# Kernel tuning notes

Hardware: AMD Instinct MI355X
Metric: run time of the kernel (lower is better)

Reference implementation:

```python
import jax, jax.numpy as jnp
import numpy as np

N_NODES = 50000
N_PAIRS = 800000
D = 64          # node feature dim
N_BASIS = 8     # basis functions per pair


def setup_inputs() -> dict:
    key = jax.random.key(0)
    k1, k2, k3, k4, k5, k6 = jax.random.split(key, 6)
    p1 = jax.random.normal(k1, (N_NODES, D), dtype=jnp.float32)
    pair_i = jax.random.randint(k2, (N_PAIRS,), 0, N_NODES, dtype=jnp.int64)
    pair_j = jax.random.randint(k3, (N_PAIRS,), 0, N_NODES, dtype=jnp.int64)
    basis = jax.random.normal(k4, (N_PAIRS, N_BASIS), dtype=jnp.float32)
    # bias-free MLP: 64 -> 256 -> 512 (= D * N_BASIS), scaled init
    W1 = jax.random.normal(k5, (D, 256), dtype=jnp.float32) / np.sqrt(D)
    W2 = jax.random.normal(k6, (256, D * N_BASIS), dtype=jnp.float32) / np.sqrt(256.0)
    return {"p1": p1, "pair_i": pair_i, "pair_j": pair_j, "basis": basis,
            "W1": W1, "W2": W2}


def reference(p1, pair_i, pair_j, basis, W1, W2):
    # gather node features for both ends of each pair and sum -> [n_pairs, D]
    inter = p1[pair_i] + p1[pair_j]
    # bias-free FeedForward with tanh between layers
    h = jnp.tanh(inter @ W1)          # [n_pairs, 256]
    h = h @ W2                        # [n_pairs, D * N_BASIS]
    h = h.reshape(-1, p1.shape[-1], basis.shape[-1])  # [n_pairs, D, n_basis]
    out = jnp.einsum('icb,ib->ic', h, basis)          # [n_pairs, D]
    return out[:, None, :]            # [n_pairs, 1, D]
```

## Files before the change

kernel.cpp:

```cpp
#include <hip/hip_runtime.h>

typedef unsigned short u16;
typedef unsigned int   u32;
typedef __bf16 bf16x8 __attribute__((ext_vector_type(8)));
typedef float  f32x4  __attribute__((ext_vector_type(4)));
typedef float  f32x2  __attribute__((ext_vector_type(2)));
typedef unsigned short u16x8 __attribute__((ext_vector_type(8)));

#define PPB 160

__device__ __forceinline__ u16 f2bf(float f){
  union { float f; u32 i; } v; v.f = f;
  u32 u = v.i;
  u += 0x7fffu + ((u >> 16) & 1u);
  return (u16)(u >> 16);
}
__device__ __forceinline__ float tanh_fast(float x){
  x = fminf(fmaxf(x, -12.f), 12.f);
  float t = __builtin_amdgcn_exp2f(x * 2.885390081777926815f);
  return (t - 1.f) * __builtin_amdgcn_rcpf(t + 1.f);
}

__global__ __launch_bounds__(256) void transpose_cast_k(
    const float* __restrict__ in, u16* __restrict__ out, int R, int C)
{
  __shared__ u16 tile[64][65];
  const int tx = threadIdx.x & 63;
  const int ty = threadIdx.x >> 6;
  const int c0 = blockIdx.x * 64;
  const int r0 = blockIdx.y * 64;
#pragma unroll
  for (int rr = 0; rr < 16; ++rr){
    int r = ty + rr * 4;
    tile[r][tx] = f2bf(in[(size_t)(r0 + r) * C + c0 + tx]);
  }
  __syncthreads();
#pragma unroll
  for (int rr = 0; rr < 16; ++rr){
    int r = ty + rr * 4;
    out[(size_t)(c0 + r) * R + r0 + tx] = tile[tx][r];
  }
}

__global__ __launch_bounds__(256) void w2_block_k(
    const float* __restrict__ in, u16* __restrict__ out)
{
  __shared__ float tile[32][65];
  const int kk = blockIdx.x;
  const int n0 = blockIdx.y * 64;
  const int t  = threadIdx.x;
  {
    int r  = t >> 3;
    int c8 = t & 7;
    const float* src = in + (size_t)(kk*32 + r)*512 + n0 + c8*8;
    f32x4 v0 = *(const f32x4*)src;
    f32x4 v1 = *(const f32x4*)(src + 4);
#pragma unroll
    for (int e = 0; e < 4; ++e){
      tile[r][c8*8 + e]     = v0[e];
      tile[r][c8*8 + 4 + e] = v1[e];
    }
  }
  __syncthreads();
  {
    int c = t >> 2, part = t & 3;
    u16x8 o;
#pragma unroll
    for (int e = 0; e < 8; ++e) o[e] = f2bf(tile[part*8 + e][c]);
    *(u16x8*)(out + ((size_t)kk*512 + n0 + c)*32 + part*8) = o;
  }
}

__global__ __launch_bounds__(512, 2) void pilayer_kernel(
    const float* __restrict__ p1,
    const int* __restrict__ pair_i,
    const int* __restrict__ pair_j,
    const float* __restrict__ basis,
    const u16* __restrict__ w1t,
    const u16* __restrict__ w2b,
    float* __restrict__ out,
    int n_pairs)
{
  extern __shared__ __align__(16) u16 smem[];
  u16* sh_h     = smem;
  u16* sh_inter = smem + PPB * 264;

  const int tid  = threadIdx.x;
  const int blk  = blockIdx.x;
  const int lane = tid & 63;
  const int w    = tid >> 6;
  const int m16  = lane & 15;
  const int q    = lane >> 4;

  bf16x8 awf[8][4];
#pragma unroll
  for (int kk = 0; kk < 8; ++kk)
#pragma unroll
    for (int nt = 0; nt < 4; ++nt)
      awf[kk][nt] = *(const bf16x8*)(
          w2b + ((size_t)kk*512 + w*64 + nt*16 + m16)*32 + q*8);
  __builtin_amdgcn_sched_barrier(0);

  for (int u = tid; u < PPB * 4; u += 512){
    int m   = u >> 2;
    int seg = u & 3;
    int p   = blk * PPB + m;
    if (p >= n_pairs) p = n_pairs - 1;
    const f32x4* pi = (const f32x4*)(p1 + (size_t)pair_i[p] * 64 + seg * 16);
    const f32x4* pj = (const f32x4*)(p1 + (size_t)pair_j[p] * 64 + seg * 16);
    f32x4 a0 = pi[0], a1 = pi[1], a2 = pi[2], a3 = pi[3];
    f32x4 b0 = pj[0], b1 = pj[1], b2 = pj[2], b3 = pj[3];
    u16x8 r0, r1;
#pragma unroll
    for (int e = 0; e < 4; ++e){
      r0[e]     = f2bf(a0[e] + b0[e]);
      r0[e + 4] = f2bf(a1[e] + b1[e]);
      r1[e]     = f2bf(a2[e] + b2[e]);
      r1[e + 4] = f2bf(a3[e] + b3[e]);
    }
    u16x8* dst = (u16x8*)(sh_inter + m * 72 + seg * 16);
    dst[0] = r0; dst[1] = r1;
  }
  __syncthreads();

  {
    bf16x8 af[2][2];
#pragma unroll
    for (int nt1 = 0; nt1 < 2; ++nt1)
#pragma unroll
      for (int kh = 0; kh < 2; ++kh)
        af[nt1][kh] = *(const bf16x8*)(
            w1t + (size_t)(w*32 + nt1*16 + m16)*64 + kh*32 + q*8);

    for (int mt1 = 0; mt1 < PPB/16; ++mt1){
      const u16* irow = sh_inter + (mt1*16 + m16)*72 + q*8;
      bf16x8 b0 = *(const bf16x8*)(irow);
      bf16x8 b1 = *(const bf16x8*)(irow + 32);
#pragma unroll
      for (int nt1 = 0; nt1 < 2; ++nt1){
        f32x4 acc = {0.f, 0.f, 0.f, 0.f};
        acc = __builtin_amdgcn_mfma_f32_16x16x32_bf16(af[nt1][0], b0, acc, 0, 0, 0);
        acc = __builtin_amdgcn_mfma_f32_16x16x32_bf16(af[nt1][1], b1, acc, 0, 0, 0);
        u32 lo = (u32)f2bf(tanh_fast(acc[0])) | ((u32)f2bf(tanh_fast(acc[1])) << 16);
        u32 hi = (u32)f2bf(tanh_fast(acc[2])) | ((u32)f2bf(tanh_fast(acc[3])) << 16);
        u32* dst = (u32*)(sh_h + (size_t)(mt1*16 + m16)*264 + w*32 + nt1*16 + q*4);
        dst[0] = lo; dst[1] = hi;
      }
    }
  }
  __syncthreads();

  for (int mt = 0; mt < PPB/16; ++mt){
    const int mg  = blk * PPB + mt*16 + m16;
    const int mgc = (mg < n_pairs) ? mg : (n_pairs - 1);
    f32x4 bb = *(const f32x4*)(basis + (size_t)mgc*8 + (q & 1)*4);

    const u16* hrow = sh_h + (size_t)(mt*16 + m16)*264 + q*8;
    f32x4 acc[4];
#pragma unroll
    for (int nt = 0; nt < 4; ++nt) acc[nt] = (f32x4){0.f, 0.f, 0.f, 0.f};

    bf16x8 bh = *(const bf16x8*)(hrow);
#pragma unroll
    for (int kk = 0; kk < 8; ++kk){
      bf16x8 bhn;
      if (kk < 7) bhn = *(const bf16x8*)(hrow + (kk + 1)*32);
#pragma unroll
      for (int nt = 0; nt < 4; ++nt)
        acc[nt] = __builtin_amdgcn_mfma_f32_16x16x32_bf16(
            awf[kk][nt], bh, acc[nt], 0, 0, 0);
      bh = bhn;
    }

#pragma unroll
    for (int nt = 0; nt < 4; ++nt){
      f32x4 a = acc[nt];
      float s = a[0]*bb[0] + a[1]*bb[1] + a[2]*bb[2] + a[3]*bb[3];
      s += __shfl_xor(s, 16);
      float v2 = __shfl_xor(s, 32);
      if (q == 0 && mg < n_pairs){
        f32x2 pk = {s, v2};
        *(f32x2*)(out + (size_t)mg*64 + w*8 + nt*2) = pk;
      }
    }
  }
}

extern "C" void kernel_launch(void* const* d_in, const int* in_sizes, int n_in,
                              void* d_out, int out_size, void* d_ws, size_t ws_size,
                              hipStream_t stream)
{
  const float* p1    = (const float*)d_in[0];
  const int*   pi    = (const int*)d_in[1];
  const int*   pj    = (const int*)d_in[2];
  const float* basis = (const float*)d_in[3];
  const float* W1    = (const float*)d_in[4];
  const float* W2    = (const float*)d_in[5];
  float* out = (float*)d_out;

  u16* w1t = (u16*)d_ws;
  u16* w2b = w1t + 64 * 256;

  const int n_pairs = in_sizes[1];
  const int lds_bytes = (PPB * 264 + PPB * 72) * (int)sizeof(u16);

  static int attr_done = 0;
  if (!attr_done){
    hipFuncSetAttribute((const void*)pilayer_kernel,
                        hipFuncAttributeMaxDynamicSharedMemorySize, lds_bytes);
    attr_done = 1;
  }

  transpose_cast_k<<<dim3(4, 1), 256, 0, stream>>>(W1, w1t, 64, 256);
  w2_block_k<<<dim3(8, 8), 256, 0, stream>>>(W2, w2b);

  const int blocks = (n_pairs + PPB - 1) / PPB;
  pilayer_kernel<<<blocks, 512, lds_bytes, stream>>>(
      p1, pi, pj, basis, w1t, w2b, out, n_pairs);
}
```

Measured before the change: 615.4 us.

## Double block to 1024 threads, halve per-wave tiles, XOR-swizzle LDS

The fused kernel moves from 512 to 1024 threads per block. Each wave now owns half as many output columns in both GEMMs, so it holds 16 W2 fragments in registers instead of 32, and the launch bounds hint at higher occupancy. The LDS row padding (264/72) is replaced by an XOR swizzle on 16-byte chunks to avoid bank conflicts while shrinking shared memory. The trade-off is that every wave re-reads the same h and inter rows from LDS, giving more LDS traffic per MFMA, and the larger block adds scheduling pressure.

```diff
diff --git a/kernel.cpp b/kernel.cpp
--- a/kernel.cpp
+++ b/kernel.cpp
@@ -6,6 +6,7 @@
 typedef float  f32x4  __attribute__((ext_vector_type(4)));
 typedef float  f32x2  __attribute__((ext_vector_type(2)));
 typedef unsigned short u16x8 __attribute__((ext_vector_type(8)));
+typedef unsigned int   u32x2 __attribute__((ext_vector_type(2)));
 
 #define PPB 160
 
@@ -71,7 +72,7 @@
   }
 }
 
-__global__ __launch_bounds__(512, 2) void pilayer_kernel(
+__global__ __launch_bounds__(1024, 4) void pilayer_kernel(
     const float* __restrict__ p1,
     const int* __restrict__ pair_i,
     const int* __restrict__ pair_j,
@@ -83,7 +84,7 @@
 {
   extern __shared__ __align__(16) u16 smem[];
   u16* sh_h     = smem;
-  u16* sh_inter = smem + PPB * 264;
+  u16* sh_inter = smem + PPB * 256;
 
   const int tid  = threadIdx.x;
   const int blk  = blockIdx.x;
@@ -91,96 +92,85 @@
   const int w    = tid >> 6;
   const int m16  = lane & 15;
   const int q    = lane >> 4;
-
-  bf16x8 awf[8][4];
+  const int sw   = m16 & 7;
+
+  bf16x8 awf[8][2];
 #pragma unroll
   for (int kk = 0; kk < 8; ++kk)
 #pragma unroll
-    for (int nt = 0; nt < 4; ++nt)
+    for (int nt = 0; nt < 2; ++nt)
       awf[kk][nt] = *(const bf16x8*)(
-          w2b + ((size_t)kk*512 + w*64 + nt*16 + m16)*32 + q*8);
+          w2b + ((size_t)kk*512 + w*32 + nt*16 + m16)*32 + q*8);
   __builtin_amdgcn_sched_barrier(0);
 
-  for (int u = tid; u < PPB * 4; u += 512){
-    int m   = u >> 2;
-    int seg = u & 3;
+  for (int u = tid; u < PPB * 8; u += 1024){
+    int m   = u >> 3;
+    int seg = u & 7;
     int p   = blk * PPB + m;
     if (p >= n_pairs) p = n_pairs - 1;
-    const f32x4* pi = (const f32x4*)(p1 + (size_t)pair_i[p] * 64 + seg * 16);
-    const f32x4* pj = (const f32x4*)(p1 + (size_t)pair_j[p] * 64 + seg * 16);
-    f32x4 a0 = pi[0], a1 = pi[1], a2 = pi[2], a3 = pi[3];
-    f32x4 b0 = pj[0], b1 = pj[1], b2 = pj[2], b3 = pj[3];
-    u16x8 r0, r1;
+    const f32x4* pi = (const f32x4*)(p1 + (size_t)pair_i[p] * 64 + seg * 8);
+    const f32x4* pj = (const f32x4*)(p1 + (size_t)pair_j[p] * 64 + seg * 8);
+    f32x4 a0 = pi[0], a1 = pi[1];
+    f32x4 c0 = pj[0], c1 = pj[1];
+    u16x8 r;
 #pragma unroll
     for (int e = 0; e < 4; ++e){
-      r0[e]     = f2bf(a0[e] + b0[e]);
-      r0[e + 4] = f2bf(a1[e] + b1[e]);
-      r1[e]     = f2bf(a2[e] + b2[e]);
-      r1[e + 4] = f2bf(a3[e] + b3[e]);
-    }
-    u16x8* dst = (u16x8*)(sh_inter + m * 72 + seg * 16);
-    dst[0] = r0; dst[1] = r1;
+      r[e]     = f2bf(a0[e] + c0[e]);
+      r[e + 4] = f2bf(a1[e] + c1[e]);
+    }
+    *(u16x8*)(sh_inter + m * 64 + ((seg ^ (m & 7)) * 8)) = r;
   }
   __syncthreads();
 
   {
-    bf16x8 af[2][2];
-#pragma unroll
-    for (int nt1 = 0; nt1 < 2; ++nt1)
-#pragma unroll
-      for (int kh = 0; kh < 2; ++kh)
-        af[nt1][kh] = *(const bf16x8*)(
-            w1t + (size_t)(w*32 + nt1*16 + m16)*64 + kh*32 + q*8);
-
+    const u16* arow = w1t + (size_t)(w*16 + m16)*64 + q*8;
+    bf16x8 af0 = *(const bf16x8*)(arow);
+    bf16x8 af1 = *(const bf16x8*)(arow + 32);
+    const int cw = (w*2 + (q >> 1)) ^ sw;
     for (int mt1 = 0; mt1 < PPB/16; ++mt1){
-      const u16* irow = sh_inter + (mt1*16 + m16)*72 + q*8;
-      bf16x8 b0 = *(const bf16x8*)(irow);
-      bf16x8 b1 = *(const bf16x8*)(irow + 32);
-#pragma unroll
-      for (int nt1 = 0; nt1 < 2; ++nt1){
-        f32x4 acc = {0.f, 0.f, 0.f, 0.f};
-        acc = __builtin_amdgcn_mfma_f32_16x16x32_bf16(af[nt1][0], b0, acc, 0, 0, 0);
-        acc = __builtin_amdgcn_mfma_f32_16x16x32_bf16(af[nt1][1], b1, acc, 0, 0, 0);
-        u32 lo = (u32)f2bf(tanh_fast(acc[0])) | ((u32)f2bf(tanh_fast(acc[1])) << 16);
-        u32 hi = (u32)f2bf(tanh_fast(acc[2])) | ((u32)f2bf(tanh_fast(acc[3])) << 16);
-        u32* dst = (u32*)(sh_h + (size_t)(mt1*16 + m16)*264 + w*32 + nt1*16 + q*4);
-        dst[0] = lo; dst[1] = hi;
-      }
+      const u16* irow = sh_inter + (size_t)(mt1*16 + m16) * 64;
+      bf16x8 b0 = *(const bf16x8*)(irow + (q ^ sw) * 8);
+      bf16x8 b1 = *(const bf16x8*)(irow + ((q + 4) ^ sw) * 8);
+      f32x4 acc = {0.f, 0.f, 0.f, 0.f};
+      acc = __builtin_amdgcn_mfma_f32_16x16x32_bf16(af0, b0, acc, 0, 0, 0);
+      acc = __builtin_amdgcn_mfma_f32_16x16x32_bf16(af1, b1, acc, 0, 0, 0);
+      u32 lo = (u32)f2bf(tanh_fast(acc[0])) | ((u32)f2bf(tanh_fast(acc[1])) << 16);
+      u32 hi = (u32)f2bf(tanh_fast(acc[2])) | ((u32)f2bf(tanh_fast(acc[3])) << 16);
+      u32x2 pk = {lo, hi};
+      *(u32x2*)(sh_h + (size_t)(mt1*16 + m16)*256 + cw*8 + (q & 1)*4) = pk;
     }
   }
   __syncthreads();
 
   for (int mt = 0; mt < PPB/16; ++mt){
-    const int mg  = blk * PPB + mt*16 + m16;
+    const int row = mt*16 + m16;
+    const int mg  = blk * PPB + row;
     const int mgc = (mg < n_pairs) ? mg : (n_pairs - 1);
     f32x4 bb = *(const f32x4*)(basis + (size_t)mgc*8 + (q & 1)*4);
 
-    const u16* hrow = sh_h + (size_t)(mt*16 + m16)*264 + q*8;
-    f32x4 acc[4];
-#pragma unroll
-    for (int nt = 0; nt < 4; ++nt) acc[nt] = (f32x4){0.f, 0.f, 0.f, 0.f};
-
-    bf16x8 bh = *(const bf16x8*)(hrow);
+    const u16* hbase = sh_h + (size_t)row * 256;
+    f32x4 acc0 = {0.f, 0.f, 0.f, 0.f};
+    f32x4 acc1 = {0.f, 0.f, 0.f, 0.f};
+
+    bf16x8 bh = *(const bf16x8*)(hbase + (q ^ sw) * 8);
 #pragma unroll
     for (int kk = 0; kk < 8; ++kk){
       bf16x8 bhn;
-      if (kk < 7) bhn = *(const bf16x8*)(hrow + (kk + 1)*32);
-#pragma unroll
-      for (int nt = 0; nt < 4; ++nt)
-        acc[nt] = __builtin_amdgcn_mfma_f32_16x16x32_bf16(
-            awf[kk][nt], bh, acc[nt], 0, 0, 0);
+      if (kk < 7) bhn = *(const bf16x8*)(hbase + ((((kk + 1)*4 + q) ^ sw) * 8));
+      acc0 = __builtin_amdgcn_mfma_f32_16x16x32_bf16(awf[kk][0], bh, acc0, 0, 0, 0);
+      acc1 = __builtin_amdgcn_mfma_f32_16x16x32_bf16(awf[kk][1], bh, acc1, 0, 0, 0);
       bh = bhn;
     }
 
 #pragma unroll
-    for (int nt = 0; nt < 4; ++nt){
-      f32x4 a = acc[nt];
+    for (int nt = 0; nt < 2; ++nt){
+      f32x4 a = (nt == 0) ? acc0 : acc1;
       float s = a[0]*bb[0] + a[1]*bb[1] + a[2]*bb[2] + a[3]*bb[3];
       s += __shfl_xor(s, 16);
       float v2 = __shfl_xor(s, 32);
       if (q == 0 && mg < n_pairs){
         f32x2 pk = {s, v2};
-        *(f32x2*)(out + (size_t)mg*64 + w*8 + nt*2) = pk;
+        *(f32x2*)(out + (size_t)mg*64 + w*4 + nt*2) = pk;
       }
     }
   }
@@ -202,7 +192,7 @@
   u16* w2b = w1t + 64 * 256;
 
   const int n_pairs = in_sizes[1];
-  const int lds_bytes = (PPB * 264 + PPB * 72) * (int)sizeof(u16);
+  const int lds_bytes = (PPB * 256 + PPB * 64) * (int)sizeof(u16);
 
   static int attr_done = 0;
   if (!attr_done){
@@ -215,6 +205,6 @@
   w2_block_k<<<dim3(8, 8), 256, 0, stream>>>(W2, w2b);
 
   const int blocks = (n_pairs + PPB - 1) / PPB;
-  pilayer_kernel<<<blocks, 512, lds_bytes, stream>>>(
+  pilayer_kernel<<<blocks, 1024, lds_bytes, stream>>>(
       p1, pi, pj, basis, w1t, w2b, out, n_pairs);
 }
```

New measurement: 585.2 us. 1.05x faster.
